# Performance work log

Measured on AMD Instinct MI355X. Metric: run time of the kernel, lower is better.

Reference implementation:

```python
import jax, jax.numpy as jnp
import numpy as np

N_NODES = 10000
N_EDGES = 160000
BATCH = 32
IN_FEAT = 64
POLY_K = 5
OUT_FEAT = 128


def setup_inputs() -> dict:
    key = jax.random.key(0)
    k_x, k_r, k_c, k_v, k_w, k_b = jax.random.split(key, 6)
    x = jax.random.normal(k_x, (BATCH, N_NODES, IN_FEAT), dtype=jnp.float32)
    lap_rows = jax.random.randint(k_r, (N_EDGES,), 0, N_NODES, dtype=jnp.int32)
    lap_cols = jax.random.randint(k_c, (N_EDGES,), 0, N_NODES, dtype=jnp.int32)
    # small values keep the degree-5 Chebyshev recurrence numerically tame
    lap_vals = jax.random.normal(k_v, (N_EDGES,), dtype=jnp.float32) * 0.05
    weight = jax.random.normal(k_w, (IN_FEAT * POLY_K, OUT_FEAT), dtype=jnp.float32) * 0.1
    bias = jax.random.normal(k_b, (1, 1, OUT_FEAT), dtype=jnp.float32) * 0.1
    return {"x": x, "lap_rows": lap_rows, "lap_cols": lap_cols,
            "lap_vals": lap_vals, "weight": weight, "bias": bias,
            "pooling_size": 4}


def _spmm(rows, cols, vals, m):
    # sparse [N,N] @ dense [N,M] via gather + segment_sum
    return jax.ops.segment_sum(vals[:, None] * m[cols], rows, num_segments=N_NODES)


def reference(x, lap_rows, lap_cols, lap_vals, weight, bias, pooling_size):
    B, N, F = x.shape
    K = POLY_K
    Fo = weight.shape[1]
    # x0: [N, F*B]
    x0 = jnp.transpose(x, (1, 2, 0)).reshape(N, F * B)
    terms = [x0]
    if K > 1:
        x1 = _spmm(lap_rows, lap_cols, lap_vals, x0)
        terms.append(x1)
        for _ in range(2, K):
            x2 = 2.0 * _spmm(lap_rows, lap_cols, lap_vals, x1) - x0
            terms.append(x2)
            x0, x1 = x1, x2
    xk = jnp.stack(terms, axis=0)                      # [K, N, F*B]
    xk = xk.reshape(K, N, F, B)
    xk = jnp.transpose(xk, (3, 1, 2, 0))               # [B, N, F, K]
    xk = xk.reshape(B * N, F * K)
    out = (xk @ weight).reshape(B, N, Fo)              # dense projection
    out = jax.nn.relu(out + bias)                      # bias + ReLU
    if pooling_size > 1:
        out = out.reshape(B, N // pooling_size, pooling_size, Fo).max(axis=2)
    return out
```

## Files before the change

### kernel.cpp

```cpp
#include <hip/hip_runtime.h>
#include <hip/hip_bf16.h>
#include <cstddef>
#include <cstdint>

#define N_NODES 10000
#define N_EDGES 160000
#define BATCH 32
#define IN_FEAT 64
#define POLY_K 5
#define OUT_FEAT 128
#define KTOT 320
#define POOLSZ 4
#define NPOOL 2500

typedef short bf16x8 __attribute__((ext_vector_type(8)));
typedef unsigned short u16x8 __attribute__((ext_vector_type(8)));
typedef float f32x4 __attribute__((ext_vector_type(4)));

__device__ __forceinline__ unsigned short f2bf(float f) {
  unsigned int u = __float_as_uint(f);
  unsigned int r = u + 0x7FFFu + ((u >> 16) & 1u);
  return (unsigned short)(r >> 16);
}
__device__ __forceinline__ float bf2f(unsigned short u) {
  return __uint_as_float(((unsigned int)u) << 16);
}


__global__ void zero_int_kernel(int* __restrict__ p, int n) {
  int i = blockIdx.x * 256 + threadIdx.x;
  if (i < n) p[i] = 0;
}

__global__ void hist_kernel(const int* __restrict__ rows, int* __restrict__ deg) {
  int e = blockIdx.x * 256 + threadIdx.x;
  if (e < N_EDGES) atomicAdd(&deg[rows[e]], 1);
}

__global__ void scan_kernel(const int* __restrict__ deg, int* __restrict__ row_start,
                            int* __restrict__ cursor) {
  __shared__ int sm[1024];
  __shared__ int carry;
  int t = threadIdx.x;
  if (t == 0) { carry = 0; row_start[0] = 0; }
  __syncthreads();
  for (int base = 0; base < N_NODES; base += 1024) {
    int idx = base + t;
    int v = (idx < N_NODES) ? deg[idx] : 0;
    sm[t] = v;
    __syncthreads();
    for (int off = 1; off < 1024; off <<= 1) {
      int xv = 0;
      if (t >= off) xv = sm[t - off];
      __syncthreads();
      sm[t] += xv;
      __syncthreads();
    }
    if (idx < N_NODES) {
      int incl = sm[t];
      row_start[idx + 1] = carry + incl;
      cursor[idx] = carry + incl - v;
    }
    __syncthreads();
    if (t == 1023) carry += sm[1023];
    __syncthreads();
  }
}

__global__ void scatter_kernel(const int* __restrict__ rows, const int* __restrict__ cols,
                               const float* __restrict__ vals, int* __restrict__ cursor,
                               int* __restrict__ csr_cols, float* __restrict__ csr_vals) {
  int e = blockIdx.x * 256 + threadIdx.x;
  if (e < N_EDGES) {
    int r = rows[e];
    int p = atomicAdd(&cursor[r], 1);
    csr_cols[p] = cols[e];
    csr_vals[p] = vals[e];
  }
}


__global__ void wpack_kernel(const float* __restrict__ weight, unsigned short* __restrict__ wpack) {
  int id = blockIdx.x * 256 + threadIdx.x;
  if (id >= 5120) return;
  int ft = id / 640;
  int c = (id / 64) % 10;
  int l = id % 64;
  int fo = ft * 16 + (l & 15);
  unsigned short v[8];
  #pragma unroll
  for (int j = 0; j < 8; ++j) {
    int k = c * 32 + ((l >> 4)) * 8 + j;
    int row = (k & 63) * POLY_K + (k >> 6);
    v[j] = f2bf(weight[row * OUT_FEAT + fo]);
  }
  ushort4* dst = (ushort4*)&wpack[(size_t)id * 8];
  dst[0] = make_ushort4(v[0], v[1], v[2], v[3]);
  dst[1] = make_ushort4(v[4], v[5], v[6], v[7]);
}


template <int BB>
__global__ __launch_bounds__(256) void transpose_kernel(const float* __restrict__ x,
                                                        unsigned short* __restrict__ t0, int b0) {
  constexpr int CB = 64 * BB;
  int n = blockIdx.x;
  int t = threadIdx.x;
  for (int i = t * 8; i < CB; i += 2048) {
    int b = i >> 6;
    int f = i & 63;
    const float* xp = &x[((size_t)(b0 + b) * N_NODES + n) * IN_FEAT + f];
    float4 v0 = *(const float4*)xp;
    float4 v1 = *(const float4*)(xp + 4);
    u16x8 o;
    o[0] = f2bf(v0.x); o[1] = f2bf(v0.y); o[2] = f2bf(v0.z); o[3] = f2bf(v0.w);
    o[4] = f2bf(v1.x); o[5] = f2bf(v1.y); o[6] = f2bf(v1.z); o[7] = f2bf(v1.w);
    *(u16x8*)&t0[(size_t)n * CB + i] = o;
  }
}


template <int BB>
__global__ __launch_bounds__(256) void spmm_kernel(const unsigned short* __restrict__ xin,
                                                   const unsigned short* __restrict__ prev,
                                                   unsigned short* __restrict__ xout,
                                                   const int* __restrict__ row_start,
                                                   const int* __restrict__ csr_cols,
                                                   const float* __restrict__ csr_vals,
                                                   float alpha, int use_prev) {
  constexpr int CB = 64 * BB;
  constexpr int NS = 16;
  constexpr int SCOLS = CB / NS;
  constexpr int LPR = SCOLS / 8;
  constexpr int RPB = 256 / LPR;
  constexpr int RB = (N_NODES + RPB - 1) / RPB;
  constexpr int PHB = RB * 8;
  int bid = blockIdx.x;
  int phase = bid / PHB;
  int rem = bid - phase * PHB;
  int xcd = rem & 7;
  int rowblk = rem >> 3;
  int slice = phase * 8 + xcd;
  int t = threadIdx.x;
  int rl = t / LPR;
  int cl = t - rl * LPR;
  int n = rowblk * RPB + rl;
  if (n >= N_NODES) return;
  int off = slice * SCOLS + cl * 8;

  int s = row_start[n];
  int e = row_start[n + 1];
  float acc[8];
  #pragma unroll
  for (int j = 0; j < 8; ++j) acc[j] = 0.f;

  int i = s;
  for (; i + 3 < e; i += 4) {
    int c0 = csr_cols[i + 0], c1 = csr_cols[i + 1];
    int c2 = csr_cols[i + 2], c3 = csr_cols[i + 3];
    float v0 = csr_vals[i + 0], v1 = csr_vals[i + 1];
    float v2 = csr_vals[i + 2], v3 = csr_vals[i + 3];
    u16x8 p0 = *(const u16x8*)&xin[(size_t)c0 * CB + off];
    u16x8 p1 = *(const u16x8*)&xin[(size_t)c1 * CB + off];
    u16x8 p2 = *(const u16x8*)&xin[(size_t)c2 * CB + off];
    u16x8 p3 = *(const u16x8*)&xin[(size_t)c3 * CB + off];
    #pragma unroll
    for (int j = 0; j < 8; ++j) {
      acc[j] = fmaf(v0, bf2f(p0[j]), acc[j]);
      acc[j] = fmaf(v1, bf2f(p1[j]), acc[j]);
      acc[j] = fmaf(v2, bf2f(p2[j]), acc[j]);
      acc[j] = fmaf(v3, bf2f(p3[j]), acc[j]);
    }
  }
  for (; i < e; ++i) {
    int c0 = csr_cols[i];
    float v0 = csr_vals[i];
    u16x8 p0 = *(const u16x8*)&xin[(size_t)c0 * CB + off];
    #pragma unroll
    for (int j = 0; j < 8; ++j) acc[j] = fmaf(v0, bf2f(p0[j]), acc[j]);
  }

  u16x8 o;
  if (use_prev) {
    u16x8 q = *(const u16x8*)&prev[(size_t)n * CB + off];
    #pragma unroll
    for (int j = 0; j < 8; ++j) o[j] = f2bf(alpha * acc[j] - bf2f(q[j]));
  } else {
    #pragma unroll
    for (int j = 0; j < 8; ++j) o[j] = f2bf(alpha * acc[j]);
  }
  *(u16x8*)&xout[(size_t)n * CB + off] = o;
}


template <int BB>
__global__ __launch_bounds__(256, 4) void gemm_mfma_kernel(const unsigned short* __restrict__ slices,
                                                           const unsigned short* __restrict__ wpack,
                                                           const float* __restrict__ bias,
                                                           float* __restrict__ out, int b0) {
  constexpr int CB = 64 * BB;
  constexpr int MB = (BB >= 16) ? 16 : BB;
  constexpr int MT = MB / 4;
  constexpr int SPAN = MB * 64;
  constexpr int ROWS = 4 * MB;
  constexpr size_t SLICE = (size_t)N_NODES * CB;
  __shared__ unsigned short A[ROWS * 320];

  int g = blockIdx.x;
  int bh = blockIdx.y;
  int t = threadIdx.x;

  constexpr int CHUNKS = ROWS * 40;
  for (int idx0 = 0; idx0 < CHUNKS; idx0 += 256) {
    int idx = idx0 + t;
    int row = idx / 40;
    int cphys = idx - row * 40;
    int clog = cphys ^ (row & 7);
    int kpoly = clog >> 3;
    int fb = (clog & 7) * 8;
    int bloc = row >> 2;
    int nd = row & 3;
    const unsigned short* gsrc = &slices[(size_t)kpoly * SLICE +
                                         (size_t)(g * POOLSZ + nd) * CB + bh * SPAN + bloc * 64 + fb];
    unsigned short* lbase = &A[(size_t)(idx0 + (t & 192)) * 8];
    __builtin_amdgcn_global_load_lds((const __attribute__((address_space(1))) unsigned int*)gsrc,
                                     (__attribute__((address_space(3))) unsigned int*)lbase,
                                     16, 0, 0);
  }
  __syncthreads();

  int w = t >> 6;
  int l = t & 63;
  int lm = l & 15;
  int q = l >> 4;
  int swz = lm & 7;

  f32x4 acc[MT][2];
  #pragma unroll
  for (int mt = 0; mt < MT; ++mt)
    #pragma unroll
    for (int fj = 0; fj < 2; ++fj) {
      acc[mt][fj][0] = 0.f; acc[mt][fj][1] = 0.f;
      acc[mt][fj][2] = 0.f; acc[mt][fj][3] = 0.f;
    }

  #pragma unroll
  for (int c = 0; c < 10; ++c) {
    bf16x8 bfrag[2];
    #pragma unroll
    for (int fj = 0; fj < 2; ++fj) {
      int fi = w * 2 + fj;
      bfrag[fj] = *(const bf16x8*)&wpack[(size_t)(((fi * 10) + c) * 64 + l) * 8];
    }
    #pragma unroll
    for (int mt = 0; mt < MT; ++mt) {
      bf16x8 afrag = *(const bf16x8*)&A[(mt * 16 + lm) * 320 + (((c * 4 + q) ^ swz) << 3)];
      acc[mt][0] = __builtin_amdgcn_mfma_f32_16x16x32_bf16(afrag, bfrag[0], acc[mt][0], 0, 0, 0);
      acc[mt][1] = __builtin_amdgcn_mfma_f32_16x16x32_bf16(afrag, bfrag[1], acc[mt][1], 0, 0, 0);
    }
  }

  #pragma unroll
  for (int fj = 0; fj < 2; ++fj) {
    int fo = (w * 2 + fj) * 16 + lm;
    float bv = bias[fo];
    #pragma unroll
    for (int mt = 0; mt < MT; ++mt) {
      float mx = fmaxf(fmaxf(acc[mt][fj][0], acc[mt][fj][1]),
                       fmaxf(acc[mt][fj][2], acc[mt][fj][3]));
      float val = fmaxf(mx + bv, 0.f);
      int b = b0 + bh * MB + mt * 4 + q;
      out[((size_t)b * NPOOL + g) * OUT_FEAT + fo] = val;
    }
  }
}


template <int BB>
static void run_pipeline(const float* x, const float* bias,
                         const int* row_start, const int* csr_cols, const float* csr_vals,
                         const unsigned short* wpack,
                         unsigned short* slices, float* out, hipStream_t stream) {
  constexpr int CB = 64 * BB;
  constexpr size_t SLICE = (size_t)N_NODES * CB;
  constexpr int LPR = (CB / 16) / 8;
  constexpr int RPB = 256 / LPR;
  constexpr int NBLK = ((N_NODES + RPB - 1) / RPB) * 16;
  constexpr int MB = (BB >= 16) ? 16 : BB;
  for (int b0 = 0; b0 < BATCH; b0 += BB) {
    transpose_kernel<BB><<<N_NODES, 256, 0, stream>>>(x, slices, b0);
    for (int k = 1; k < POLY_K; ++k) {
      const unsigned short* xin  = slices + (size_t)(k - 1) * SLICE;
      const unsigned short* prev = (k >= 2) ? slices + (size_t)(k - 2) * SLICE : slices;
      unsigned short* xout = slices + (size_t)k * SLICE;
      float alpha = (k == 1) ? 1.0f : 2.0f;
      spmm_kernel<BB><<<NBLK, 256, 0, stream>>>(xin, prev, xout, row_start,
                                                csr_cols, csr_vals, alpha,
                                                (k >= 2) ? 1 : 0);
    }
    gemm_mfma_kernel<BB><<<dim3(NPOOL, BB / MB), 256, 0, stream>>>(slices, wpack, bias, out, b0);
  }
}

static size_t needed_bytes(int BB) {
  return 1482112u + (size_t)6400000 * BB;
}

extern "C" void kernel_launch(void* const* d_in, const int* in_sizes, int n_in,
                              void* d_out, int out_size, void* d_ws, size_t ws_size,
                              hipStream_t stream) {
  const float* x        = (const float*)d_in[0];
  const int*   lap_rows = (const int*)d_in[1];
  const int*   lap_cols = (const int*)d_in[2];
  const float* lap_vals = (const float*)d_in[3];
  const float* weight   = (const float*)d_in[4];
  const float* bias     = (const float*)d_in[5];
  float* out = (float*)d_out;

  int* deg       = (int*)d_ws;
  int* cursor    = deg + 10016;
  int* row_start = cursor + 10016;
  int* csr_cols  = row_start + 10016;
  float* csr_vals = (float*)(csr_cols + N_EDGES);
  unsigned short* wpack = (unsigned short*)(csr_vals + N_EDGES);
  unsigned short* slices = wpack + 40960;

  int BB = 0;
  if      (ws_size >= needed_bytes(32)) BB = 32;
  else if (ws_size >= needed_bytes(16)) BB = 16;
  else if (ws_size >= needed_bytes(8))  BB = 8;
  else if (ws_size >= needed_bytes(4))  BB = 4;
  if (BB == 0) return;

  zero_int_kernel<<<(N_NODES + 255) / 256, 256, 0, stream>>>(deg, N_NODES);
  hist_kernel<<<(N_EDGES + 255) / 256, 256, 0, stream>>>(lap_rows, deg);
  scan_kernel<<<1, 1024, 0, stream>>>(deg, row_start, cursor);
  scatter_kernel<<<(N_EDGES + 255) / 256, 256, 0, stream>>>(lap_rows, lap_cols, lap_vals,
                                                            cursor, csr_cols, csr_vals);
  wpack_kernel<<<20, 256, 0, stream>>>(weight, wpack);

  switch (BB) {
    case 32: run_pipeline<32>(x, bias, row_start, csr_cols, csr_vals, wpack, slices, out, stream); break;
    case 16: run_pipeline<16>(x, bias, row_start, csr_cols, csr_vals, wpack, slices, out, stream); break;
    case 8:  run_pipeline<8>(x, bias, row_start, csr_cols, csr_vals, wpack, slices, out, stream); break;
    case 4:  run_pipeline<4>(x, bias, row_start, csr_cols, csr_vals, wpack, slices, out, stream); break;
  }
}
```

Before: 464.2 us.

## Store Chebyshev terms in column-sliced layout for contiguous SpMM gathers

Each Chebyshev term buffer is now split into NSL column slices, each stored as a contiguous [N_NODES, SCOLS] block, instead of one [N_NODES, CB] row-major array. The transpose, SpMM and GEMM kernels are all rewritten to index this layout, so each SpMM slice gathers from a compact region whose rows are SCOLS wide. The goal is better cache locality and L2 reuse for the random-neighbour gathers, since each XCD slice now touches a smaller working set. The GEMM loads become more scattered across slice blocks, which could cost some efficiency in the load-to-LDS path.

```diff
diff --git a/kernel.cpp b/kernel.cpp
--- a/kernel.cpp
+++ b/kernel.cpp
@@ -12,6 +12,7 @@
 #define KTOT 320
 #define POOLSZ 4
 #define NPOOL 2500
+#define NSL 16
 
 typedef short bf16x8 __attribute__((ext_vector_type(8)));
 typedef unsigned short u16x8 __attribute__((ext_vector_type(8)));
@@ -104,6 +105,8 @@
 __global__ __launch_bounds__(256) void transpose_kernel(const float* __restrict__ x,
                                                         unsigned short* __restrict__ t0, int b0) {
   constexpr int CB = 64 * BB;
+  constexpr int SCOLS = CB / NSL;
+  constexpr size_t SLICE_SL = (size_t)N_NODES * SCOLS;
   int n = blockIdx.x;
   int t = threadIdx.x;
   for (int i = t * 8; i < CB; i += 2048) {
@@ -115,7 +118,9 @@
     u16x8 o;
     o[0] = f2bf(v0.x); o[1] = f2bf(v0.y); o[2] = f2bf(v0.z); o[3] = f2bf(v0.w);
     o[4] = f2bf(v1.x); o[5] = f2bf(v1.y); o[6] = f2bf(v1.z); o[7] = f2bf(v1.w);
-    *(u16x8*)&t0[(size_t)n * CB + i] = o;
+    int sl = i / SCOLS;
+    int cw = i & (SCOLS - 1);
+    *(u16x8*)&t0[(size_t)sl * SLICE_SL + (size_t)n * SCOLS + cw] = o;
   }
 }
 
@@ -129,8 +134,8 @@
                                                    const float* __restrict__ csr_vals,
                                                    float alpha, int use_prev) {
   constexpr int CB = 64 * BB;
-  constexpr int NS = 16;
-  constexpr int SCOLS = CB / NS;
+  constexpr int SCOLS = CB / NSL;
+  constexpr size_t SLICE_SL = (size_t)N_NODES * SCOLS;
   constexpr int LPR = SCOLS / 8;
   constexpr int RPB = 256 / LPR;
   constexpr int RB = (N_NODES + RPB - 1) / RPB;
@@ -146,7 +151,11 @@
   int cl = t - rl * LPR;
   int n = rowblk * RPB + rl;
   if (n >= N_NODES) return;
-  int off = slice * SCOLS + cl * 8;
+  int off = cl * 8;
+
+  const unsigned short* xs = xin  + (size_t)slice * SLICE_SL;
+  const unsigned short* ps = prev + (size_t)slice * SLICE_SL;
+  unsigned short*       os = xout + (size_t)slice * SLICE_SL;
 
   int s = row_start[n];
   int e = row_start[n + 1];
@@ -160,10 +169,10 @@
     int c2 = csr_cols[i + 2], c3 = csr_cols[i + 3];
     float v0 = csr_vals[i + 0], v1 = csr_vals[i + 1];
     float v2 = csr_vals[i + 2], v3 = csr_vals[i + 3];
-    u16x8 p0 = *(const u16x8*)&xin[(size_t)c0 * CB + off];
-    u16x8 p1 = *(const u16x8*)&xin[(size_t)c1 * CB + off];
-    u16x8 p2 = *(const u16x8*)&xin[(size_t)c2 * CB + off];
-    u16x8 p3 = *(const u16x8*)&xin[(size_t)c3 * CB + off];
+    u16x8 p0 = *(const u16x8*)&xs[(size_t)c0 * SCOLS + off];
+    u16x8 p1 = *(const u16x8*)&xs[(size_t)c1 * SCOLS + off];
+    u16x8 p2 = *(const u16x8*)&xs[(size_t)c2 * SCOLS + off];
+    u16x8 p3 = *(const u16x8*)&xs[(size_t)c3 * SCOLS + off];
     #pragma unroll
     for (int j = 0; j < 8; ++j) {
       acc[j] = fmaf(v0, bf2f(p0[j]), acc[j]);
@@ -175,21 +184,21 @@
   for (; i < e; ++i) {
     int c0 = csr_cols[i];
     float v0 = csr_vals[i];
-    u16x8 p0 = *(const u16x8*)&xin[(size_t)c0 * CB + off];
+    u16x8 p0 = *(const u16x8*)&xs[(size_t)c0 * SCOLS + off];
     #pragma unroll
     for (int j = 0; j < 8; ++j) acc[j] = fmaf(v0, bf2f(p0[j]), acc[j]);
   }
 
   u16x8 o;
   if (use_prev) {
-    u16x8 q = *(const u16x8*)&prev[(size_t)n * CB + off];
+    u16x8 q = *(const u16x8*)&ps[(size_t)n * SCOLS + off];
     #pragma unroll
     for (int j = 0; j < 8; ++j) o[j] = f2bf(alpha * acc[j] - bf2f(q[j]));
   } else {
     #pragma unroll
     for (int j = 0; j < 8; ++j) o[j] = f2bf(alpha * acc[j]);
   }
-  *(u16x8*)&xout[(size_t)n * CB + off] = o;
+  *(u16x8*)&os[(size_t)n * SCOLS + off] = o;
 }
 
 
@@ -199,11 +208,12 @@
                                                            const float* __restrict__ bias,
                                                            float* __restrict__ out, int b0) {
   constexpr int CB = 64 * BB;
+  constexpr int SCOLS = CB / NSL;
+  constexpr size_t SLICE_SL = (size_t)N_NODES * SCOLS;
   constexpr int MB = (BB >= 16) ? 16 : BB;
   constexpr int MT = MB / 4;
   constexpr int SPAN = MB * 64;
   constexpr int ROWS = 4 * MB;
-  constexpr size_t SLICE = (size_t)N_NODES * CB;
   __shared__ unsigned short A[ROWS * 320];
 
   int g = blockIdx.x;
@@ -220,8 +230,11 @@
     int fb = (clog & 7) * 8;
     int bloc = row >> 2;
     int nd = row & 3;
-    const unsigned short* gsrc = &slices[(size_t)kpoly * SLICE +
-                                         (size_t)(g * POOLSZ + nd) * CB + bh * SPAN + bloc * 64 + fb];
+    int c = bh * SPAN + bloc * 64 + fb;
+    int sl = c / SCOLS;
+    int cw = c & (SCOLS - 1);
+    const unsigned short* gsrc = &slices[((size_t)kpoly * NSL + sl) * SLICE_SL +
+                                         (size_t)(g * POOLSZ + nd) * SCOLS + cw];
     unsigned short* lbase = &A[(size_t)(idx0 + (t & 192)) * 8];
     __builtin_amdgcn_global_load_lds((const __attribute__((address_space(1))) unsigned int*)gsrc,
                                      (__attribute__((address_space(3))) unsigned int*)lbase,
@@ -282,17 +295,17 @@
                          const unsigned short* wpack,
                          unsigned short* slices, float* out, hipStream_t stream) {
   constexpr int CB = 64 * BB;
-  constexpr size_t SLICE = (size_t)N_NODES * CB;
-  constexpr int LPR = (CB / 16) / 8;
+  constexpr size_t TERM = (size_t)N_NODES * CB;
+  constexpr int LPR = (CB / NSL) / 8;
   constexpr int RPB = 256 / LPR;
-  constexpr int NBLK = ((N_NODES + RPB - 1) / RPB) * 16;
+  constexpr int NBLK = ((N_NODES + RPB - 1) / RPB) * NSL;
   constexpr int MB = (BB >= 16) ? 16 : BB;
   for (int b0 = 0; b0 < BATCH; b0 += BB) {
     transpose_kernel<BB><<<N_NODES, 256, 0, stream>>>(x, slices, b0);
     for (int k = 1; k < POLY_K; ++k) {
-      const unsigned short* xin  = slices + (size_t)(k - 1) * SLICE;
-      const unsigned short* prev = (k >= 2) ? slices + (size_t)(k - 2) * SLICE : slices;
-      unsigned short* xout = slices + (size_t)k * SLICE;
+      const unsigned short* xin  = slices + (size_t)(k - 1) * TERM;
+      const unsigned short* prev = (k >= 2) ? slices + (size_t)(k - 2) * TERM : slices;
+      unsigned short* xout = slices + (size_t)k * TERM;
       float alpha = (k == 1) ? 1.0f : 2.0f;
       spmm_kernel<BB><<<NBLK, 256, 0, stream>>>(xin, prev, xout, row_start,
                                                 csr_cols, csr_vals, alpha,
```

Result: faster. 444.1 us (-4.3%).
